# Kernel tuning notes

Hardware: AMD Instinct MI355X
Metric: run time of the kernel (lower is better)

The kernel has to match this reference:

```python
import jax, jax.numpy as jnp
import numpy as np

B, T, D = 2, 2048, 2048
H, KV = 32, 8
HD = D // H            # 64
N_REP = H // KV        # 4


def setup_inputs() -> dict:
    key = jax.random.key(0)
    ks = jax.random.split(key, 5)
    x = jax.random.normal(ks[0], (B, T, D), dtype=jnp.float32)
    # RoPE frequencies: angle[t, i] = t / 10000^(2i/HD), i in [0, HD/2)
    inv_freq = 1.0 / (10000.0 ** (jnp.arange(0, HD, 2, dtype=jnp.float32) / HD))
    ang = jnp.arange(T, dtype=jnp.float32)[:, None] * inv_freq[None, :]  # [T, HD/2]
    freqs_cos = jnp.cos(ang)
    freqs_sin = jnp.sin(ang)
    # causal additive mask [1,1,T,T]
    r = jnp.arange(T)
    mask = jnp.where(r[None, :] > r[:, None], -1e9, 0.0).astype(jnp.float32)[None, None]
    s = 0.02
    wq = jax.random.normal(ks[1], (D, H * HD), dtype=jnp.float32) * s
    wk = jax.random.normal(ks[2], (D, KV * HD), dtype=jnp.float32) * s
    wv = jax.random.normal(ks[3], (D, KV * HD), dtype=jnp.float32) * s
    wo = jax.random.normal(ks[4], (H * HD, D), dtype=jnp.float32) * s
    return {"x": x, "freqs_cos": freqs_cos, "freqs_sin": freqs_sin, "mask": mask,
            "wq": wq, "wk": wk, "wv": wv, "wo": wo}


def _rope(t, cos, sin):
    # t: [B, T, h, HD]; complex rotation on consecutive (even, odd) pairs
    t2 = t.reshape(*t.shape[:-1], HD // 2, 2)
    c = cos[None, :, None, :]
    s = sin[None, :, None, :]
    o0 = t2[..., 0] * c - t2[..., 1] * s
    o1 = t2[..., 0] * s + t2[..., 1] * c
    return jnp.stack([o0, o1], axis=-1).reshape(t.shape)


def reference(x, freqs_cos, freqs_sin, mask, wq, wk, wv, wo):
    q = (x @ wq).reshape(B, T, H, HD)
    k = (x @ wk).reshape(B, T, KV, HD)
    v = (x @ wv).reshape(B, T, KV, HD)
    q = _rope(q, freqs_cos, freqs_sin)
    k = _rope(k, freqs_cos, freqs_sin)
    # GQA expand: each kv head repeated N_REP times consecutively
    k = jnp.repeat(k, N_REP, axis=2)  # [B, T, H, HD]
    v = jnp.repeat(v, N_REP, axis=2)
    scores = jnp.einsum('bqhd,bkhd->bhqk', q, k) / jnp.sqrt(jnp.float32(HD))
    scores = scores + mask
    attn = jax.nn.softmax(scores, axis=-1)
    out = jnp.einsum('bhqk,bkhd->bqhd', attn, v).reshape(B, T, H * HD)
    return out @ wo
```

## Files before the change

### kernel.cpp

```cpp
#include <hip/hip_runtime.h>
#include <hip/hip_bf16.h>

#define T_SEQ 2048
#define NROWS 4096
#define QKS   2560

typedef __attribute__((ext_vector_type(8))) short short8;
typedef __attribute__((ext_vector_type(4))) float f32x4;
typedef __attribute__((ext_vector_type(16))) float f32x16;
typedef __attribute__((ext_vector_type(2))) int i32x2;
typedef __attribute__((ext_vector_type(2))) unsigned int u32x2;

#define KC 0.18033688f

__device__ __forceinline__ unsigned short f2bf(float f) {
    unsigned u = __builtin_bit_cast(unsigned, f);
    u += 0x7FFF + ((u >> 16) & 1);
    return (unsigned short)(u >> 16);
}
__device__ __forceinline__ float bf2f(unsigned short s) {
    unsigned u = ((unsigned)s) << 16;
    return __builtin_bit_cast(float, u);
}

__device__ __forceinline__ void gload_lds16(const void* g, void* l) {
    __builtin_amdgcn_global_load_lds(
        (const __attribute__((address_space(1))) unsigned int*)g,
        (__attribute__((address_space(3))) unsigned int*)l,
        16, 0, 0);
}

__device__ __forceinline__ f32x4 mfma16(short8 a, short8 b, f32x4 c) {
    return __builtin_amdgcn_mfma_f32_16x16x32_bf16(a, b, c, 0, 0, 0);
}
__device__ __forceinline__ f32x16 mfma32(short8 a, short8 b, f32x16 c) {
    return __builtin_amdgcn_mfma_f32_32x32x16_bf16(a, b, c, 0, 0, 0);
}

__device__ __forceinline__ unsigned cvtpk_bf16(float lo, float hi) {
    unsigned r;
    asm("v_cvt_pk_bf16_f32 %0, %1, %2" : "=v"(r) : "v"(lo), "v"(hi));
    return r;
}

__device__ __forceinline__ short8 frag_from_u32(unsigned w0, unsigned w1, unsigned w2, unsigned w3) {
    union { unsigned u[4]; short8 s; } t;
    t.u[0] = w0; t.u[1] = w1; t.u[2] = w2; t.u[3] = w3;
    return t.s;
}

__global__ __launch_bounds__(256) void prep(const float* __restrict__ x,
                                            const float* __restrict__ wq,
                                            const float* __restrict__ wk,
                                            const float* __restrict__ wv,
                                            short* __restrict__ xb,
                                            short* __restrict__ wT) {
    __shared__ float tile[32][33];
    const int bid = blockIdx.x, t = threadIdx.x;
    if (bid < 4096) {
        const int i = bid * 256 + t;
        const float4 a = ((const float4*)x)[i * 2];
        const float4 b = ((const float4*)x)[i * 2 + 1];
        ((short8*)xb)[i] = frag_from_u32(cvtpk_bf16(a.x, a.y), cvtpk_bf16(a.z, a.w),
                                         cvtpk_bf16(b.x, b.y), cvtpk_bf16(b.z, b.w));
        return;
    }
    const int r = bid - 4096;
    const int bx = r % 96, by = r / 96;
    const float* S; int srcN, nt, dstRow0;
    if (bx < 64)      { S = wq; srcN = 2048; nt = bx;      dstRow0 = 0;    }
    else if (bx < 80) { S = wk; srcN = 512;  nt = bx - 64; dstRow0 = 2048; }
    else              { S = wv; srcN = 512;  nt = bx - 80; dstRow0 = 2560; }
    const int n0 = nt * 32, k0 = by * 32;
#pragma unroll
    for (int j = 0; j < 4; ++j) {
        int lin = t + 256 * j;
        int kk = lin >> 5, nn = lin & 31;
        tile[kk][nn] = S[(size_t)(k0 + kk) * srcN + n0 + nn];
    }
    __syncthreads();
#pragma unroll
    for (int j = 0; j < 4; ++j) {
        int lin = t + 256 * j;
        int nn = lin >> 5, kk = lin & 31;
        wT[(size_t)(dstRow0 + n0 + nn) * 2048 + k0 + kk] = (short)f2bf(tile[kk][nn]);
    }
}

__global__ __launch_bounds__(256) void transpose_f32_bf16(const float* __restrict__ S,
                                                          short* __restrict__ D,
                                                          int K, int N) {
    __shared__ float tile[32][33];
    const int n0 = blockIdx.x * 32, k0 = blockIdx.y * 32;
    const int t = threadIdx.x;
#pragma unroll
    for (int j = 0; j < 4; ++j) {
        int lin = t + 256 * j;
        int kk = lin >> 5, nn = lin & 31;
        tile[kk][nn] = S[(size_t)(k0 + kk) * N + n0 + nn];
    }
    __syncthreads();
#pragma unroll
    for (int j = 0; j < 4; ++j) {
        int lin = t + 256 * j;
        int nn = lin >> 5, kk = lin & 31;
        D[(size_t)(n0 + nn) * K + k0 + kk] = (short)f2bf(tile[kk][nn]);
    }
}

__global__ __launch_bounds__(256) void rope_vt(unsigned short* __restrict__ qk,
                                               const float* __restrict__ cosp,
                                               const float* __restrict__ sinp,
                                               const short* __restrict__ vbuf,
                                               short* __restrict__ vt) {
    __shared__ short tile[32][33];
    const int bid = blockIdx.x, t = threadIdx.x;
    if (bid < 2048) {
        const int c0 = (bid & 15) * 32, r0 = (bid >> 4) * 32;
#pragma unroll
        for (int j = 0; j < 4; ++j) {
            int lin = t + 256 * j;
            int rr = lin >> 5, cc = lin & 31;
            tile[rr][cc] = vbuf[(size_t)(r0 + rr) * 512 + c0 + cc];
        }
        __syncthreads();
#pragma unroll
        for (int j = 0; j < 4; ++j) {
            int lin = t + 256 * j;
            int cc = lin >> 5, rr = lin & 31;
            vt[(size_t)(c0 + cc) * NROWS + r0 + rr] = tile[rr][cc];
        }
        return;
    }
    int i = (bid - 2048) * 256 + t;
    int Hn = 32, c0 = 0;
    if (i >= 2097152) { i -= 2097152; Hn = 8; c0 = 2048; }
    const int gp = i * 2;
    const int p = gp & 31;
    const int hh = (gp >> 5) % Hn;
    const int row = gp / (32 * Hn);
    const int tpos = row & (T_SEQ - 1);
    const float2 cw = *(const float2*)(cosp + tpos * 32 + p);
    const float2 sw = *(const float2*)(sinp + tpos * 32 + p);
    const size_t base = (size_t)row * QKS + c0 + hh * 64 + 2 * p;
    u32x2 v = *(u32x2*)(qk + base);
    const float e0 = bf2f((unsigned short)(v.x & 0xFFFF)), o0 = bf2f((unsigned short)(v.x >> 16));
    const float e1 = bf2f((unsigned short)(v.y & 0xFFFF)), o1 = bf2f((unsigned short)(v.y >> 16));
    v.x = cvtpk_bf16(e0 * cw.x - o0 * sw.x, e0 * sw.x + o0 * cw.x);
    v.y = cvtpk_bf16(e1 * cw.y - o1 * sw.y, e1 * sw.y + o1 * cw.y);
    *(u32x2*)(qk + base) = v;
}

template <int STORE_F32>
__global__ __launch_bounds__(256) void gemm_mfma(const short* __restrict__ A,
                                                 const short* __restrict__ Bt,
                                                 void* __restrict__ C, int ldc,
                                                 short* __restrict__ Cv, int nsplit,
                                                 int M, int N, int K) {
    __shared__ short As[2][128 * 32];
    __shared__ short Bs[2][128 * 32];
    const int tid = threadIdx.x;
    const int l = tid & 63, w = tid >> 6;
    const int wr = w >> 1, wc = w & 1;
    const int lm = l & 15, lg = l >> 4;

    const int nwg = gridDim.x * gridDim.y;
    int bid = blockIdx.y * gridDim.x + blockIdx.x;
    bid = (bid & 7) * (nwg >> 3) + (bid >> 3);
    const int row0 = (bid / gridDim.x) * 128;
    const int col0 = (bid % gridDim.x) * 128;

    f32x4 acc[4][4];
#pragma unroll
    for (int m = 0; m < 4; ++m)
#pragma unroll
        for (int n = 0; n < 4; ++n) acc[m][n] = (f32x4){0.f, 0.f, 0.f, 0.f};

    auto STAGE = [&](int buf, int kt) {
        const int k0 = kt * 32;
#pragma unroll
        for (int p = 0; p < 2; ++p) {
            const int c = tid + 256 * p;
            const int r = c >> 2, k8 = (c & 3) * 8;
            gload_lds16(A  + (size_t)(row0 + r) * K + k0 + k8, &As[buf][c * 8]);
            gload_lds16(Bt + (size_t)(col0 + r) * K + k0 + k8, &Bs[buf][c * 8]);
        }
    };

    const int nk = K >> 5;
    STAGE(0, 0);
    asm volatile("s_waitcnt vmcnt(0)" ::: "memory");
    __syncthreads();

    for (int kt = 0; kt < nk; ++kt) {
        const int cur = kt & 1;
        if (kt + 1 < nk) STAGE(cur ^ 1, kt + 1);

        short8 af[4], bfr[4];
#pragma unroll
        for (int m = 0; m < 4; ++m)
            af[m] = *(const short8*)(&As[cur][(wr * 64 + m * 16 + lm) * 32 + lg * 8]);
#pragma unroll
        for (int n = 0; n < 4; ++n)
            bfr[n] = *(const short8*)(&Bs[cur][(wc * 64 + n * 16 + lm) * 32 + lg * 8]);
#pragma unroll
        for (int m = 0; m < 4; ++m)
#pragma unroll
            for (int n = 0; n < 4; ++n)
                acc[m][n] = mfma16(af[m], bfr[n], acc[m][n]);

        asm volatile("s_waitcnt vmcnt(0)" ::: "memory");
        __syncthreads();
    }

    const bool vreg = (!STORE_F32) && (col0 >= nsplit);
#pragma unroll
    for (int m = 0; m < 4; ++m)
#pragma unroll
        for (int n = 0; n < 4; ++n) {
            if (vreg) {
#pragma unroll
                for (int r = 0; r < 4; ++r) {
                    const int row = row0 + wr * 64 + m * 16 + lg * 4 + r;
                    const int col = col0 + wc * 64 + n * 16 + lm - nsplit;
                    Cv[(size_t)row * 512 + col] = (short)f2bf(acc[m][n][r]);
                }
            } else {
#pragma unroll
                for (int r = 0; r < 4; ++r) {
                    const int row = row0 + wr * 64 + m * 16 + lg * 4 + r;
                    const int col = col0 + wc * 64 + n * 16 + lm;
                    const float v = acc[m][n][r];
                    if (STORE_F32) ((float*)C)[(size_t)row * ldc + col] = v;
                    else ((unsigned short*)C)[(size_t)row * ldc + col] = f2bf(v);
                }
            }
        }
}

template <int STORE_F32>
__global__ __launch_bounds__(256) void gemm64(const short* __restrict__ A,
                                              const short* __restrict__ Bt,
                                              void* __restrict__ C, int ldc,
                                              short* __restrict__ Cv, int nsplit,
                                              int M, int N, int K) {
    __shared__ short As[2][128 * 64];
    __shared__ short Bs[2][128 * 64];
    const int tid = threadIdx.x;
    const int l = tid & 63, w = tid >> 6;
    const int wr = w >> 1, wc = w & 1;
    const int lm = l & 15, lg = l >> 4;

    const int nwg = gridDim.x * gridDim.y;
    int bid = blockIdx.y * gridDim.x + blockIdx.x;
    bid = (bid & 7) * (nwg >> 3) + (bid >> 3);
    const int row0 = (bid / gridDim.x) * 128;
    const int col0 = (bid % gridDim.x) * 128;

    f32x4 acc[4][4];
#pragma unroll
    for (int m = 0; m < 4; ++m)
#pragma unroll
        for (int n = 0; n < 4; ++n) acc[m][n] = (f32x4){0.f, 0.f, 0.f, 0.f};

    auto STAGE = [&](int buf, int kt) {
        const int k0 = kt * 64;
#pragma unroll
        for (int p = 0; p < 4; ++p) {
            const int c = tid + 256 * p;
            const int r = c >> 3, s = c & 7;
            const int gs = s ^ (r & 7);
            gload_lds16(A  + (size_t)(row0 + r) * K + k0 + gs * 8, &As[buf][c * 8]);
            gload_lds16(Bt + (size_t)(col0 + r) * K + k0 + gs * 8, &Bs[buf][c * 8]);
        }
    };

    const int nk = K >> 6;
    STAGE(0, 0);
    asm volatile("s_waitcnt vmcnt(0)" ::: "memory");
    __syncthreads();

    for (int kt = 0; kt < nk; ++kt) {
        const int cur = kt & 1;
        if (kt + 1 < nk) STAGE(cur ^ 1, kt + 1);

#pragma unroll
        for (int kh = 0; kh < 2; ++kh) {
            short8 af[4], bfr[4];
#pragma unroll
            for (int m = 0; m < 4; ++m) {
                const int r = wr * 64 + m * 16 + lm;
                const int s = (kh * 4 + lg) ^ (r & 7);
                af[m] = *(const short8*)(&As[cur][r * 64 + s * 8]);
            }
#pragma unroll
            for (int n = 0; n < 4; ++n) {
                const int r = wc * 64 + n * 16 + lm;
                const int s = (kh * 4 + lg) ^ (r & 7);
                bfr[n] = *(const short8*)(&Bs[cur][r * 64 + s * 8]);
            }
#pragma unroll
            for (int m = 0; m < 4; ++m)
#pragma unroll
                for (int n = 0; n < 4; ++n)
                    acc[m][n] = mfma16(af[m], bfr[n], acc[m][n]);
        }

        asm volatile("s_waitcnt vmcnt(0)" ::: "memory");
        __syncthreads();
    }

    const bool vreg = (!STORE_F32) && (col0 >= nsplit);
#pragma unroll
    for (int m = 0; m < 4; ++m)
#pragma unroll
        for (int n = 0; n < 4; ++n) {
            if (vreg) {
#pragma unroll
                for (int r = 0; r < 4; ++r) {
                    const int row = row0 + wr * 64 + m * 16 + lg * 4 + r;
                    const int col = col0 + wc * 64 + n * 16 + lm - nsplit;
                    Cv[(size_t)row * 512 + col] = (short)f2bf(acc[m][n][r]);
                }
            } else {
#pragma unroll
                for (int r = 0; r < 4; ++r) {
                    const int row = row0 + wr * 64 + m * 16 + lg * 4 + r;
                    const int col = col0 + wc * 64 + n * 16 + lm;
                    const float v = acc[m][n][r];
                    if (STORE_F32) ((float*)C)[(size_t)row * ldc + col] = v;
                    else ((unsigned short*)C)[(size_t)row * ldc + col] = f2bf(v);
                }
            }
        }
}

__global__ __launch_bounds__(256, 4) void attn_fwd(const short* __restrict__ qkv,
                                                   const short* __restrict__ vt,
                                                   unsigned short* __restrict__ aout) {
    __shared__ short Ks[2][64 * 64];
    __shared__ short Vs[2][64 * 64];
    const int bid = blockIdx.x;
    const int q2 = (bid & 3) ^ ((bid >> 8) & 3);
    const int t  = (bid >> 2) & 15;
    const int gb = ((bid >> 6) & 3) | (((bid >> 8) & 3) << 2);
    const int qt = (q2 == 0) ? t : (q2 == 1) ? (31 - t) : (q2 == 2) ? (32 + t) : (63 - t);
    const int g = gb & 7, b = gb >> 3;

    const int tid = threadIdx.x, l = tid & 63, w = tid >> 6;
    const int n = l & 31, hi = l >> 5;
    const int h = g * 4 + w;
    const int Q0 = qt * 32;
    const int qg = Q0 + n;

    const size_t krow_base = (size_t)(b * T_SEQ) * QKS + 2048 + g * 64;
    const size_t vrow_base = (size_t)(g * 64) * NROWS + b * T_SEQ;

    short8 qb[4];
    {
        const size_t qbase = (size_t)(b * T_SEQ + qg) * QKS + h * 64 + hi * 8;
        qb[0] = *(const short8*)(qkv + qbase);
        qb[1] = *(const short8*)(qkv + qbase + 16);
        qb[2] = *(const short8*)(qkv + qbase + 32);
        qb[3] = *(const short8*)(qkv + qbase + 48);
    }

    f32x16 acc0 = {}, acc1 = {};
    float m_run = -1e30f, l_run = 0.f;

    const int ntiles = (qt >> 1) + 1;

    auto STAGE = [&](int buf, int kt) {
        const int krow0 = kt * 64;
#pragma unroll
        for (int p = 0; p < 2; ++p) {
            const int c = p * 256 + tid;
            const int r = c >> 3, gk = c & 7;
            const int gs = gk ^ (r & 7);
            gload_lds16(qkv + krow_base + (size_t)(krow0 + r) * QKS + gs * 8,
                        &Ks[buf][c * 8]);
            gload_lds16(vt + vrow_base + (size_t)r * NROWS + krow0 + gs * 8,
                        &Vs[buf][c * 8]);
        }
    };

    STAGE(0, 0);
    asm volatile("s_waitcnt vmcnt(0)" ::: "memory");
    __syncthreads();

    for (int kt = 0; kt < ntiles; ++kt) {
        const int cur = kt & 1;
        if (kt + 1 < ntiles) STAGE(cur ^ 1, kt + 1);

        const int krow0 = kt * 64;
        const short* KsB = &Ks[cur][0];
        const short* VsB = &Vs[cur][0];

        f32x16 s0 = {}, s1 = {};
        __builtin_amdgcn_s_setprio(1);
#pragma unroll
        for (int ks = 0; ks < 4; ++ks) {
            const int perm = ((2 * ks + hi) ^ (n & 7)) * 8;
            const short8 kf0 = *(const short8*)(KsB + n * 64 + perm);
            const short8 kf1 = *(const short8*)(KsB + (32 + n) * 64 + perm);
            s0 = mfma32(kf0, qb[ks], s0);
            s1 = mfma32(kf1, qb[ks], s1);
        }
        __builtin_amdgcn_s_setprio(0);

        if (krow0 + 63 > Q0) {
#pragma unroll
            for (int r = 0; r < 16; ++r) {
                const int jj = krow0 + (r & 3) + 8 * (r >> 2) + 4 * hi;
                if (jj > qg) s0[r] = -1e30f;
                if (jj + 32 > qg) s1[r] = -1e30f;
            }
        }

        float t8[8];
#pragma unroll
        for (int r = 0; r < 8; ++r)
            t8[r] = fmaxf(fmaxf(s0[r], s0[r + 8]), fmaxf(s1[r], s1[r + 8]));
        float mx = fmaxf(fmaxf(fmaxf(t8[0], t8[1]), fmaxf(t8[2], t8[3])),
                         fmaxf(fmaxf(t8[4], t8[5]), fmaxf(t8[6], t8[7])));
        mx = fmaxf(mx, __shfl_xor(mx, 32));
        const float pm = mx * KC;

        if (!__all(pm <= m_run + 8.0f)) {
            const float mn = fmaxf(m_run, pm);
            const float sc = __builtin_amdgcn_exp2f(m_run - mn);
            l_run *= sc;
#pragma unroll
            for (int r = 0; r < 16; ++r) { acc0[r] *= sc; acc1[r] *= sc; }
            m_run = mn;
        }

        float ps[4] = {0.f, 0.f, 0.f, 0.f};
#pragma unroll
        for (int r = 0; r < 16; ++r) {
            const float p = __builtin_amdgcn_exp2f(__builtin_fmaf(s0[r], KC, -m_run));
            s0[r] = p; ps[r & 3] += p;
        }
#pragma unroll
        for (int r = 0; r < 16; ++r) {
            const float p = __builtin_amdgcn_exp2f(__builtin_fmaf(s1[r], KC, -m_run));
            s1[r] = p; ps[r & 3] += p;
        }
        float pst = (ps[0] + ps[1]) + (ps[2] + ps[3]);
        pst += __shfl_xor(pst, 32);
        l_run += pst;

        __builtin_amdgcn_s_setprio(1);
#define PV_STEP(KS, SV)                                                              \
        {                                                                            \
            const unsigned c01 = cvtpk_bf16(SV[((KS)&1)*8+0], SV[((KS)&1)*8+1]);     \
            const unsigned c23 = cvtpk_bf16(SV[((KS)&1)*8+2], SV[((KS)&1)*8+3]);     \
            const unsigned c45 = cvtpk_bf16(SV[((KS)&1)*8+4], SV[((KS)&1)*8+5]);     \
            const unsigned c67 = cvtpk_bf16(SV[((KS)&1)*8+6], SV[((KS)&1)*8+7]);     \
            const i32x2 r02 = __builtin_amdgcn_permlane32_swap((int)c01, (int)c45, false, false); \
            const i32x2 r13 = __builtin_amdgcn_permlane32_swap((int)c23, (int)c67, false, false); \
            const short8 pfrag = frag_from_u32((unsigned)r02.x, (unsigned)r13.x,     \
                                               (unsigned)r02.y, (unsigned)r13.y);    \
            const int permv = ((2 * (KS) + hi) ^ (n & 7)) * 8;                       \
            const short8 vf0 = *(const short8*)(VsB + n * 64 + permv);               \
            const short8 vf1 = *(const short8*)(VsB + (32 + n) * 64 + permv);        \
            acc0 = mfma32(vf0, pfrag, acc0);                                         \
            acc1 = mfma32(vf1, pfrag, acc1);                                         \
        }
        PV_STEP(0, s0)
        PV_STEP(1, s0)
        PV_STEP(2, s1)
        PV_STEP(3, s1)
#undef PV_STEP
        __builtin_amdgcn_s_setprio(0);

        asm volatile("s_waitcnt vmcnt(0)" ::: "memory");
        __syncthreads();
    }

    const float invl = 1.0f / l_run;
    const size_t orow = (size_t)(b * T_SEQ + qg) * 2048 + h * 64;
#pragma unroll
    for (int rg = 0; rg < 4; ++rg) {
        u32x2 pk0, pk1;
        pk0.x = cvtpk_bf16(acc0[rg * 4 + 0] * invl, acc0[rg * 4 + 1] * invl);
        pk0.y = cvtpk_bf16(acc0[rg * 4 + 2] * invl, acc0[rg * 4 + 3] * invl);
        pk1.x = cvtpk_bf16(acc1[rg * 4 + 0] * invl, acc1[rg * 4 + 1] * invl);
        pk1.y = cvtpk_bf16(acc1[rg * 4 + 2] * invl, acc1[rg * 4 + 3] * invl);
        *(u32x2*)(aout + orow + rg * 8 + hi * 4) = pk0;
        *(u32x2*)(aout + orow + 32 + rg * 8 + hi * 4) = pk1;
    }
}

extern "C" void kernel_launch(void* const* d_in, const int* in_sizes, int n_in,
                              void* d_out, int out_size, void* d_ws, size_t ws_size,
                              hipStream_t stream) {
    const float* x    = (const float*)d_in[0];
    const float* fcos = (const float*)d_in[1];
    const float* fsin = (const float*)d_in[2];
    const float* wq   = (const float*)d_in[4];
    const float* wk   = (const float*)d_in[5];
    const float* wv   = (const float*)d_in[6];
    const float* wo   = (const float*)d_in[7];

    short* ws0  = (short*)d_ws;
    short* qkvb = ws0;
    short* vt   = ws0 + 10485760;
    short* wT   = ws0 + 12582912;
    short* vbuf = ws0 + 18874368;
    short* aout = ws0 + 12582912;
    short* woT  = ws0;
    short* xb   = (short*)d_out;

    prep<<<10240, 256, 0, stream>>>(x, wq, wk, wv, xb, wT);
    gemm_mfma<0><<<dim3(24, 32), 256, 0, stream>>>(xb, wT, qkvb, QKS, vbuf, 2560,
                                                   NROWS, 3072, 2048);
    rope_vt<<<12288, 256, 0, stream>>>((unsigned short*)qkvb, fcos, fsin, vbuf, vt);
    attn_fwd<<<1024, 256, 0, stream>>>(qkvb, vt, (unsigned short*)aout);
    transpose_f32_bf16<<<dim3(64, 64), 256, 0, stream>>>(wo, woT, 2048, 2048);
    gemm64<1><<<dim3(16, 32), 256, 0, stream>>>(aout, woT, d_out, 2048, nullptr, 1 << 30,
                                                NROWS, 2048, 2048);
}
```

Before: 200.0 us.

## Fuse RoPE into QKV GEMM epilogue and double attention query tile per block

Applies RoPE inside the QKV GEMM epilogue, using a lane shuffle to fetch the paired even/odd element, so the separate rope pass over Q and K in global memory is no longer needed; the leftover kernel only transposes V. The attention kernel now runs 512-thread blocks covering 64 query rows (two 32-row halves sharing each K/V tile), which halves the number of blocks and the K/V staging traffic per query row. The trade-offs are extra cos/sin loads and shuffles in the GEMM epilogue, coarser load balance across the causal triangle, and heavier register and LDS pressure per block.

```diff
diff --git a/kernel.cpp b/kernel.cpp
--- a/kernel.cpp
+++ b/kernel.cpp
@@ -108,54 +108,33 @@
     }
 }
 
-__global__ __launch_bounds__(256) void rope_vt(unsigned short* __restrict__ qk,
-                                               const float* __restrict__ cosp,
-                                               const float* __restrict__ sinp,
-                                               const short* __restrict__ vbuf,
+__global__ __launch_bounds__(256) void vt_only(const short* __restrict__ vbuf,
                                                short* __restrict__ vt) {
     __shared__ short tile[32][33];
     const int bid = blockIdx.x, t = threadIdx.x;
-    if (bid < 2048) {
-        const int c0 = (bid & 15) * 32, r0 = (bid >> 4) * 32;
-#pragma unroll
-        for (int j = 0; j < 4; ++j) {
-            int lin = t + 256 * j;
-            int rr = lin >> 5, cc = lin & 31;
-            tile[rr][cc] = vbuf[(size_t)(r0 + rr) * 512 + c0 + cc];
-        }
-        __syncthreads();
-#pragma unroll
-        for (int j = 0; j < 4; ++j) {
-            int lin = t + 256 * j;
-            int cc = lin >> 5, rr = lin & 31;
-            vt[(size_t)(c0 + cc) * NROWS + r0 + rr] = tile[rr][cc];
-        }
-        return;
-    }
-    int i = (bid - 2048) * 256 + t;
-    int Hn = 32, c0 = 0;
-    if (i >= 2097152) { i -= 2097152; Hn = 8; c0 = 2048; }
-    const int gp = i * 2;
-    const int p = gp & 31;
-    const int hh = (gp >> 5) % Hn;
-    const int row = gp / (32 * Hn);
-    const int tpos = row & (T_SEQ - 1);
-    const float2 cw = *(const float2*)(cosp + tpos * 32 + p);
-    const float2 sw = *(const float2*)(sinp + tpos * 32 + p);
-    const size_t base = (size_t)row * QKS + c0 + hh * 64 + 2 * p;
-    u32x2 v = *(u32x2*)(qk + base);
-    const float e0 = bf2f((unsigned short)(v.x & 0xFFFF)), o0 = bf2f((unsigned short)(v.x >> 16));
-    const float e1 = bf2f((unsigned short)(v.y & 0xFFFF)), o1 = bf2f((unsigned short)(v.y >> 16));
-    v.x = cvtpk_bf16(e0 * cw.x - o0 * sw.x, e0 * sw.x + o0 * cw.x);
-    v.y = cvtpk_bf16(e1 * cw.y - o1 * sw.y, e1 * sw.y + o1 * cw.y);
-    *(u32x2*)(qk + base) = v;
-}
-
-template <int STORE_F32>
+    const int c0 = (bid & 15) * 32, r0 = (bid >> 4) * 32;
+#pragma unroll
+    for (int j = 0; j < 4; ++j) {
+        int lin = t + 256 * j;
+        int rr = lin >> 5, cc = lin & 31;
+        tile[rr][cc] = vbuf[(size_t)(r0 + rr) * 512 + c0 + cc];
+    }
+    __syncthreads();
+#pragma unroll
+    for (int j = 0; j < 4; ++j) {
+        int lin = t + 256 * j;
+        int cc = lin >> 5, rr = lin & 31;
+        vt[(size_t)(c0 + cc) * NROWS + r0 + rr] = tile[rr][cc];
+    }
+}
+
+template <int STORE_F32, int ROPE>
 __global__ __launch_bounds__(256) void gemm_mfma(const short* __restrict__ A,
                                                  const short* __restrict__ Bt,
                                                  void* __restrict__ C, int ldc,
                                                  short* __restrict__ Cv, int nsplit,
+                                                 const float* __restrict__ cosp,
+                                                 const float* __restrict__ sinp,
                                                  int M, int N, int K) {
     __shared__ short As[2][128 * 32];
     __shared__ short Bs[2][128 * 32];
@@ -214,6 +193,7 @@
     }
 
     const bool vreg = (!STORE_F32) && (col0 >= nsplit);
+    const bool dorope = ROPE && (col0 < 2560);
 #pragma unroll
     for (int m = 0; m < 4; ++m)
 #pragma unroll
@@ -226,11 +206,20 @@
                     Cv[(size_t)row * 512 + col] = (short)f2bf(acc[m][n][r]);
                 }
             } else {
+                const int p = (n * 16 + lm) >> 1;
 #pragma unroll
                 for (int r = 0; r < 4; ++r) {
                     const int row = row0 + wr * 64 + m * 16 + lg * 4 + r;
                     const int col = col0 + wc * 64 + n * 16 + lm;
-                    const float v = acc[m][n][r];
+                    float v = acc[m][n][r];
+                    if (dorope) {
+                        const int tpos = row & (T_SEQ - 1);
+                        const float cc = cosp[tpos * 32 + p];
+                        const float ss = sinp[tpos * 32 + p];
+                        const float pw = __shfl_xor(v, 1);
+                        v = (lm & 1) ? __builtin_fmaf(pw, ss, v * cc)
+                                     : __builtin_fmaf(v, cc, -(pw * ss));
+                    }
                     if (STORE_F32) ((float*)C)[(size_t)row * ldc + col] = v;
                     else ((unsigned short*)C)[(size_t)row * ldc + col] = f2bf(v);
                 }
@@ -335,22 +324,22 @@
         }
 }
 
-__global__ __launch_bounds__(256, 4) void attn_fwd(const short* __restrict__ qkv,
+__global__ __launch_bounds__(512, 4) void attn_fwd(const short* __restrict__ qkv,
                                                    const short* __restrict__ vt,
                                                    unsigned short* __restrict__ aout) {
     __shared__ short Ks[2][64 * 64];
     __shared__ short Vs[2][64 * 64];
     const int bid = blockIdx.x;
-    const int q2 = (bid & 3) ^ ((bid >> 8) & 3);
-    const int t  = (bid >> 2) & 15;
-    const int gb = ((bid >> 6) & 3) | (((bid >> 8) & 3) << 2);
-    const int qt = (q2 == 0) ? t : (q2 == 1) ? (31 - t) : (q2 == 2) ? (32 + t) : (63 - t);
-    const int g = gb & 7, b = gb >> 3;
+    const int t = (bid >> 1) & 15;
+    const int gbb = (bid >> 5) & 15;
+    const int h1 = (bid & 1) ^ ((bid >> 8) & 1);
+    const int qt = h1 ? (31 - t) : t;
+    const int g = gbb & 7, b = gbb >> 3;
 
     const int tid = threadIdx.x, l = tid & 63, w = tid >> 6;
     const int n = l & 31, hi = l >> 5;
-    const int h = g * 4 + w;
-    const int Q0 = qt * 32;
+    const int h = g * 4 + (w & 3);
+    const int Q0 = qt * 64 + (w >> 2) * 32;
     const int qg = Q0 + n;
 
     const size_t krow_base = (size_t)(b * T_SEQ) * QKS + 2048 + g * 64;
@@ -368,20 +357,17 @@
     f32x16 acc0 = {}, acc1 = {};
     float m_run = -1e30f, l_run = 0.f;
 
-    const int ntiles = (qt >> 1) + 1;
+    const int ntiles = qt + 1;
 
     auto STAGE = [&](int buf, int kt) {
         const int krow0 = kt * 64;
-#pragma unroll
-        for (int p = 0; p < 2; ++p) {
-            const int c = p * 256 + tid;
-            const int r = c >> 3, gk = c & 7;
-            const int gs = gk ^ (r & 7);
-            gload_lds16(qkv + krow_base + (size_t)(krow0 + r) * QKS + gs * 8,
-                        &Ks[buf][c * 8]);
-            gload_lds16(vt + vrow_base + (size_t)r * NROWS + krow0 + gs * 8,
-                        &Vs[buf][c * 8]);
-        }
+        const int c = tid;
+        const int r = c >> 3, gk = c & 7;
+        const int gs = gk ^ (r & 7);
+        gload_lds16(qkv + krow_base + (size_t)(krow0 + r) * QKS + gs * 8,
+                    &Ks[buf][c * 8]);
+        gload_lds16(vt + vrow_base + (size_t)r * NROWS + krow0 + gs * 8,
+                    &Vs[buf][c * 8]);
     };
 
     STAGE(0, 0);
@@ -513,10 +499,10 @@
     short* xb   = (short*)d_out;
 
     prep<<<10240, 256, 0, stream>>>(x, wq, wk, wv, xb, wT);
-    gemm_mfma<0><<<dim3(24, 32), 256, 0, stream>>>(xb, wT, qkvb, QKS, vbuf, 2560,
-                                                   NROWS, 3072, 2048);
-    rope_vt<<<12288, 256, 0, stream>>>((unsigned short*)qkvb, fcos, fsin, vbuf, vt);
-    attn_fwd<<<1024, 256, 0, stream>>>(qkvb, vt, (unsigned short*)aout);
+    gemm_mfma<0, 1><<<dim3(24, 32), 256, 0, stream>>>(xb, wT, qkvb, QKS, vbuf, 2560,
+                                                      fcos, fsin, NROWS, 3072, 2048);
+    vt_only<<<2048, 256, 0, stream>>>(vbuf, vt);
+    attn_fwd<<<512, 512, 0, stream>>>(qkvb, vt, (unsigned short*)aout);
     transpose_f32_bf16<<<dim3(64, 64), 256, 0, stream>>>(wo, woT, 2048, 2048);
     gemm64<1><<<dim3(16, 32), 256, 0, stream>>>(aout, woT, d_out, 2048, nullptr, 1 << 30,
                                                 NROWS, 2048, 2048);
```

Result: no change. 199.9 us (-0.0%).
